# Kernel tuning notes

Hardware: AMD Instinct MI355X
Metric: run time of the kernel (lower is better)

The kernel has to match this reference:

```python
import jax, jax.numpy as jnp
import numpy as np

# EEACSF hyperparameters (module defaults)
CUTOFF = 5.2
ANG_CUTOFF = 3.5
RADIAL_ETA = 16.0
ANGULAR_ETA = 8.0
RDIV = 16          # radial_dist_divisions
ADIV = 4           # angular_dist_divisions
ZETA = 32.0
SECTIONS = 4       # angle_sections
R_START = 0.8
A_START = 0.8
N_SPECIES = 87     # size of periodic-table / valence table

N_ATOMS = 20000
N_EDGES = 640000       # radial edges
N_ANG_EDGES = 160000   # angular-graph edges
N_PAIRS = 560000       # angle pairs


def setup_inputs() -> dict:
    key = jax.random.key(0)
    ks = jax.random.split(key, 12)
    species = jax.random.randint(ks[0], (N_ATOMS,), 0, N_SPECIES)
    # radial graph: distances in (R_START, CUTOFF)
    distances = R_START + (CUTOFF - R_START) * jax.random.uniform(ks[1], (N_EDGES,), jnp.float32)
    switch = jax.random.uniform(ks[2], (N_EDGES,), jnp.float32)
    edge_src = jax.random.randint(ks[3], (N_EDGES,), 0, N_ATOMS)
    edge_dst = jax.random.randint(ks[4], (N_EDGES,), 0, N_ATOMS)
    # angular graph
    ang_angles = np.pi * jax.random.uniform(ks[5], (N_PAIRS,), jnp.float32)
    ang_distances = A_START + (ANG_CUTOFF - A_START) * jax.random.uniform(ks[6], (N_ANG_EDGES,), jnp.float32)
    ang_switch = jax.random.uniform(ks[7], (N_ANG_EDGES,), jnp.float32)
    ang_edge_dst = jax.random.randint(ks[8], (N_ANG_EDGES,), 0, N_ATOMS)
    angle_src = jax.random.randint(ks[9], (N_PAIRS,), 0, N_ANG_EDGES)
    angle_dst = jax.random.randint(ks[10], (N_PAIRS,), 0, N_ANG_EDGES)
    central_atom = jax.random.randint(ks[11], (N_PAIRS,), 0, N_ATOMS)
    # valence structure table (stands in for the preprocessed VALENCE_STRUCTURE constant)
    valence_table = jax.random.uniform(jax.random.fold_in(key, 99), (N_SPECIES, 4), jnp.float32)
    return {
        "species": species, "distances": distances, "switch": switch,
        "edge_src": edge_src, "edge_dst": edge_dst,
        "ang_angles": ang_angles, "ang_distances": ang_distances,
        "ang_switch": ang_switch, "ang_edge_dst": ang_edge_dst,
        "angle_src": angle_src, "angle_dst": angle_dst,
        "central_atom": central_atom, "valence_table": valence_table,
    }


def reference(species, distances, switch, edge_src, edge_dst,
              ang_angles, ang_distances, ang_switch, ang_edge_dst,
              angle_src, angle_dst, central_atom, valence_table):
    n_atoms = species.shape[0]
    valence = valence_table[species]                                  # [N,4]

    # ---- radial AEV ----
    shiftR = jnp.asarray(np.linspace(R_START, CUTOFF, RDIV + 1)[None, :-1], distances.dtype)
    x2 = RADIAL_ETA * (distances[:, None] - shiftR) ** 2              # [E,16]
    radial_terms = 0.25 * jnp.exp(-x2) * switch[:, None]              # [E,16]
    radial_aev = jax.ops.segment_sum(
        radial_terms[:, :, None] * valence[edge_dst, None, :],        # [E,16,4]
        edge_src, num_segments=n_atoms,
    ).reshape(n_atoms, -1)                                            # [N,64]

    # ---- angular AEV ----
    d12 = 0.5 * (ang_distances[angle_src] + ang_distances[angle_dst])[:, None]  # [P,1]
    angle_start = np.pi / (2 * SECTIONS)
    shiftZ = jnp.asarray((np.linspace(0, np.pi, SECTIONS + 1) + angle_start)[None, :-1], ang_distances.dtype)
    shiftA = jnp.asarray(np.linspace(A_START, ANG_CUTOFF, ADIV + 1)[None, :-1], ang_distances.dtype)
    factor1 = (0.5 + 0.5 * jnp.cos(ang_angles[:, None] - shiftZ)) ** ZETA       # [P,4]
    factor2 = jnp.exp(-ANGULAR_ETA * (d12 - shiftA) ** 2)                       # [P,4]
    angular_terms = (factor1[:, None, :] * factor2[:, :, None]).reshape(-1, SECTIONS * ADIV)
    angular_terms = angular_terms * 2 * (ang_switch[angle_src] * ang_switch[angle_dst])[:, None]  # [P,16]

    valence_dst = valence[ang_edge_dst]                               # [E2,4]
    vp = valence_dst[angle_src] + valence_dst[angle_dst]              # [P,4]
    vm = valence_dst[angle_src] * valence_dst[angle_dst]              # [P,4]
    valence_ang = (vp[:, :, None] * vm[:, None, :]).reshape(-1, 16)   # [P,16]

    angular_aev = jax.ops.segment_sum(
        angular_terms[:, :, None] * valence_ang[:, None, :],          # [P,16,16]
        central_atom, num_segments=n_atoms,
    ).reshape(n_atoms, -1)                                            # [N,256]

    onehot = jax.nn.one_hot(species, N_SPECIES, dtype=distances.dtype)  # [N,87]
    return jnp.concatenate((onehot, radial_aev, angular_aev), axis=-1)  # [N,407]
```

## Files before the change

### kernel.cpp

```cpp
#include <hip/hip_runtime.h>
#include <hip/hip_fp16.h>
#include <math.h>

#define NCOLS   407
#define RAD_OFF 87
#define ANG_OFF 151
#define T1      3072
#define KPT     (T1 / 256)
#define WB      32
#define MAXBKT  640
#define CAPF    1792
#define C2      (CAPF / 256)


typedef __attribute__((ext_vector_type(8))) _Float16 f16x8;
typedef __attribute__((ext_vector_type(4))) float    f32x4;

static __device__ inline unsigned pack2(float a, float b) {
    __half2 h = __floats2half2_rn(a, b);
    return *reinterpret_cast<unsigned*>(&h);
}
static __device__ inline float2 unpack2(unsigned u) {
    __half2 h = *reinterpret_cast<__half2*>(&u);
    return __half22float2(h);
}

__global__ __launch_bounds__(256) void ze_kernel(const float* __restrict__ ang_dist,
                                                 const float* __restrict__ ang_sw,
                                                 const int* __restrict__ ang_edge_dst,
                                                 const float* __restrict__ dist,
                                                 const float* __restrict__ sw,
                                                 const int* __restrict__ edst,
                                                 const int* __restrict__ species,
                                                 const float4* __restrict__ valence,
                                                 uint4* __restrict__ edata,
                                                 uint4* __restrict__ rad_edata,
                                                 int* __restrict__ cursors,
                                                 int n_ang_edges, int n_edges,
                                                 int nbe, int nbr) {
    int bid = blockIdx.x;
    int t = threadIdx.x;
    if (bid == nbe + nbr) {
        for (int i = t; i < 2 * MAXBKT; i += 256) cursors[i] = 0;
        return;
    }
    if (bid < nbe) {
        int i = bid * 2560 + t;
        #pragma unroll
        for (int k = 0; k < 10; ++k, i += 256) {
            if (i < n_ang_edges) {
                float4 v = valence[species[ang_edge_dst[i]]];
                uint4 r;
                r.x = __float_as_uint(ang_dist[i]);
                r.y = __float_as_uint(ang_sw[i]);
                r.z = pack2(v.x, v.y);
                r.w = pack2(v.z, v.w);
                edata[i] = r;
            }
        }
    } else {
        int i = (bid - nbe) * 2560 + t;
        #pragma unroll
        for (int k = 0; k < 10; ++k, i += 256) {
            if (i < n_edges) {
                float d  = dist[i];
                float ps = 0.25f * sw[i];
                float4 v = valence[species[edst[i]]];
                uint4 r;
                r.x = __float_as_uint(d);
                r.y = pack2(ps * v.x, ps * v.y);
                r.z = pack2(ps * v.z, ps * v.w);
                r.w = 0u;
                rad_edata[i] = r;
            }
        }
    }
}

__global__ __launch_bounds__(256) void pass1_kernel(
    const uint4* __restrict__ rad_edata,
    const int* __restrict__ esrc,
    const float* __restrict__ ang_angles,
    const int* __restrict__ psrc, const int* __restrict__ pdst,
    const int* __restrict__ central,
    int* __restrict__ cur_rad, int* __restrict__ cur_ang,
    uint4* __restrict__ arr_rad, uint4* __restrict__ arr_ang,
    int n_edges, int n_pairs, int nbkt, int nt_rad)
{
    __shared__ uint4 buf[T1];
    __shared__ int   lh[MAXBKT];
    __shared__ int   gb[MAXBKT];
    __shared__ int   wtot[4];

    int bid = blockIdx.x;
    int t = threadIdx.x;
    int is_ang = bid >= nt_rad;
    const int* key = is_ang ? central : esrc;
    int* cursor = is_ang ? cur_ang : cur_rad;
    int n   = is_ang ? n_pairs : n_edges;
    int off = (is_ang ? bid - nt_rad : bid) * T1;
    int cnt = min(T1, n - off);
    uint4* arr = is_ang ? arr_ang : arr_rad;

    for (int b = t; b < nbkt; b += 256) lh[b] = 0;
    __syncthreads();

    int meta[KPT];
    #pragma unroll
    for (int k = 0; k < KPT; ++k) {
        int i = off + k * 256 + t;
        meta[k] = -1;
        if (i < n) {
            int atom = key[i];
            int r = atomicAdd(&lh[atom >> 5], 1);
            meta[k] = (atom << 12) | r;
        }
    }
    __syncthreads();

    {
        int w = t >> 6, lane = t & 63;
        int W4  = (nbkt + 3) >> 2;
        int wlo = w * W4;
        int whi = min(wlo + W4, nbkt);
        int b0 = wlo + lane * 3;
        int c0 = (b0     < whi) ? lh[b0]     : 0;
        int c1 = (b0 + 1 < whi) ? lh[b0 + 1] : 0;
        int c2 = (b0 + 2 < whi) ? lh[b0 + 2] : 0;
        int lsum = c0 + c1 + c2;
        int s = lsum;
        #pragma unroll
        for (int o = 1; o < 64; o <<= 1) {
            int u = __shfl_up(s, o, 64);
            if (lane >= o) s += u;
        }
        int excl = s - lsum;
        if (c0) gb[b0]     = b0       * CAPF + atomicAdd(&cursor[b0],     c0);
        if (c1) gb[b0 + 1] = (b0 + 1) * CAPF + atomicAdd(&cursor[b0 + 1], c1);
        if (c2) gb[b0 + 2] = (b0 + 2) * CAPF + atomicAdd(&cursor[b0 + 2], c2);
        if (b0     < whi) lh[b0]     = excl;
        if (b0 + 1 < whi) lh[b0 + 1] = excl + c0;
        if (b0 + 2 < whi) lh[b0 + 2] = excl + c0 + c1;
        if (lane == 63) wtot[w] = s;
        __syncthreads();
        int wbase = 0;
        for (int ww = 0; ww < w; ++ww) wbase += wtot[ww];
        if (wbase) {
            if (b0     < whi) lh[b0]     += wbase;
            if (b0 + 1 < whi) lh[b0 + 1] += wbase;
            if (b0 + 2 < whi) lh[b0 + 2] += wbase;
        }
        __syncthreads();
    }

    #pragma unroll
    for (int k = 0; k < KPT; ++k) {
        if (meta[k] < 0) continue;
        int i = off + k * 256 + t;
        int atom = meta[k] >> 12, r = meta[k] & 4095;
        int b = atom >> 5;
        uint4 rec;
        if (!is_ang) {
            uint4 e = rad_edata[i];
            rec.x = e.x; rec.y = e.y; rec.z = e.z;
            rec.w = (unsigned)atom;
        } else {
            rec.x = (unsigned)psrc[i];
            rec.y = (unsigned)pdst[i];
            rec.z = __float_as_uint(ang_angles[i]);
            rec.w = (unsigned)atom;
        }
        buf[lh[b] + r] = rec;
    }
    __syncthreads();

    #pragma unroll
    for (int k = 0; k < KPT; ++k) {
        int j = k * 256 + t;
        if (j < cnt) {
            uint4 r = buf[j];
            int b = (int)(r.w >> 5);
            int gpos = gb[b] + (j - lh[b]);
            if (gpos < (b + 1) * CAPF) arr[gpos] = r;
        }
    }
}

__global__ __launch_bounds__(256) void pass2B_kernel(
    const uint4* __restrict__ arr_rad, const uint4* __restrict__ arr_ang,
    const uint4* __restrict__ edata,
    const int* __restrict__ cur_rad, const int* __restrict__ cur_ang,
    const int* __restrict__ species,
    float* __restrict__ out, int nbkt, int n_atoms)
{
    __shared__ uint4 buf[CAPF];
    __shared__ unsigned short ord[CAPF];
    __shared__ int lh[WB];
    __shared__ int sA[WB + 1];
    __shared__ uint4 stg[4][256];

    int bid = blockIdx.x;
    int t = threadIdx.x;
    int g = bid >= nbkt;
    int b = g ? bid - nbkt : bid;
    int lo  = b * CAPF;
    int cnt = min(g ? cur_ang[b] : cur_rad[b], CAPF);
    const uint4* arr = g ? arr_ang : arr_rad;
    int loA = b << 5;

    if (t < WB) lh[t] = 0;
    __syncthreads();
    int myar[C2];
    #pragma unroll
    for (int c = 0; c < C2; ++c) {
        int j = c * 256 + t;
        myar[c] = -1;
        if (j < cnt) {
            uint4 r = arr[lo + j];
            buf[j] = r;
            int a = (int)r.w - loA;
            if ((unsigned)a < WB) {
                int rk = atomicAdd(&lh[a], 1);
                myar[c] = (a << 12) | rk;
            }
        }
    }
    __syncthreads();
    if (t < 64) {
        int v = (t < WB) ? lh[t] : 0;
        int s = v;
        #pragma unroll
        for (int o = 1; o < WB; o <<= 1) {
            int u = __shfl_up(s, o, 64);
            if (t >= o) s += u;
        }
        if (t < WB) sA[t + 1] = s;
        if (t == 0) sA[0] = 0;
    }
    __syncthreads();
    #pragma unroll
    for (int c = 0; c < C2; ++c) {
        if (myar[c] >= 0) {
            int j = c * 256 + t;
            ord[sA[myar[c] >> 12] + (myar[c] & 4095)] = (unsigned short)j;
        }
    }
    __syncthreads();

    int w    = t >> 6;
    int lane = t & 63;
    int m  = lane & 15;
    int g4 = lane >> 4;

    if (g) {
        const _Float16* hl = (const _Float16*)stg[w];
        for (int ai = 0; ai < 8; ++ai) {
            int a = w * 8 + ai;
            int atom = loA + a;
            if (atom >= n_atoms) break;
            int beg = sA[a], end = sA[a + 1];
            f32x4 acc = {0.f, 0.f, 0.f, 0.f};

            for (int base = beg; base < end; base += 64) {
                int idx = base + lane;
                unsigned q[16];
                if (idx < end) {
                    uint4 pr = buf[ord[idx]];
                    int e1 = (int)pr.x;
                    int e2 = (int)pr.y;
                    float ang = __uint_as_float(pr.z);
                    uint4 r1 = edata[e1];
                    uint4 r2 = edata[e2];
                    float d12 = 0.5f * (__uint_as_float(r1.x) + __uint_as_float(r2.x));
                    float swp = 2.0f * __uint_as_float(r1.y) * __uint_as_float(r2.y);
                    float2 v1a = unpack2(r1.z), v1b = unpack2(r1.w);
                    float2 v2a = unpack2(r2.z), v2b = unpack2(r2.w);
                    float vp[4] = {v1a.x + v2a.x, v1a.y + v2a.y, v1b.x + v2b.x, v1b.y + v2b.y};
                    float vm[4] = {v1a.x * v2a.x, v1a.y * v2a.y, v1b.x * v2b.x, v1b.y * v2b.y};

                    float sa, ca;
                    __sincosf(ang, &sa, &ca);
                    const float czv[4] = { 0.92387953f,  0.38268343f, -0.38268343f, -0.92387953f };
                    const float szv[4] = { 0.38268343f,  0.92387953f,  0.92387953f,  0.38268343f };
                    float f1v[4];
                    #pragma unroll
                    for (int z = 0; z < 4; ++z) {
                        float y = 0.5f + 0.5f * (ca * czv[z] + sa * szv[z]);
                        float y2 = y * y, y4 = y2 * y2, y8 = y4 * y4, y16 = y8 * y8;
                        f1v[z] = y16 * y16;
                    }
                    float f2sv[4];
                    #pragma unroll
                    for (int aa = 0; aa < 4; ++aa) {
                        float x = d12 - (0.8f + 0.675f * (float)aa);
                        f2sv[aa] = swp * __expf(-8.0f * x * x);
                    }
                    #pragma unroll
                    for (int aa = 0; aa < 4; ++aa) {
                        q[aa * 2 + 0] = pack2(f2sv[aa] * f1v[0], f2sv[aa] * f1v[1]);
                        q[aa * 2 + 1] = pack2(f2sv[aa] * f1v[2], f2sv[aa] * f1v[3]);
                    }
                    #pragma unroll
                    for (int i2 = 0; i2 < 4; ++i2) {
                        q[8 + i2 * 2 + 0] = pack2(vp[i2] * vm[0], vp[i2] * vm[1]);
                        q[8 + i2 * 2 + 1] = pack2(vp[i2] * vm[2], vp[i2] * vm[3]);
                    }
                } else {
                    #pragma unroll
                    for (int k = 0; k < 16; ++k) q[k] = 0u;
                }
                stg[w][lane * 4 + 0] = make_uint4(q[0],  q[1],  q[2],  q[3]);
                stg[w][lane * 4 + 1] = make_uint4(q[4],  q[5],  q[6],  q[7]);
                stg[w][lane * 4 + 2] = make_uint4(q[8],  q[9],  q[10], q[11]);
                stg[w][lane * 4 + 3] = make_uint4(q[12], q[13], q[14], q[15]);
                asm volatile("s_waitcnt lgkmcnt(0)" ::: "memory");

                int cc = min(64, end - base);
                {
                    f16x8 wf, uf;
                    #pragma unroll
                    for (int i = 0; i < 8; ++i) {
                        int row = (g4 << 3) + i;
                        wf[i] = hl[row * 32 + m];
                        uf[i] = hl[row * 32 + 16 + m];
                    }
                    acc = __builtin_amdgcn_mfma_f32_16x16x32_f16(wf, uf, acc, 0, 0, 0);
                }
                if (cc > 32) {
                    f16x8 wf, uf;
                    #pragma unroll
                    for (int i = 0; i < 8; ++i) {
                        int row = 32 + (g4 << 3) + i;
                        wf[i] = hl[row * 32 + m];
                        uf[i] = hl[row * 32 + 16 + m];
                    }
                    acc = __builtin_amdgcn_mfma_f32_16x16x32_f16(wf, uf, acc, 0, 0, 0);
                }
                asm volatile("s_waitcnt lgkmcnt(0)" ::: "memory");
            }
            float* orow = out + (size_t)atom * NCOLS + ANG_OFF;
            #pragma unroll
            for (int r = 0; r < 4; ++r)
                orow[(g4 * 4 + r) * 16 + m] = acc[r];
        }
        return;
    }

    const _Float16* hl = (const _Float16*)buf;
    const float*    fl = (const float*)buf;
    float shiftm = 0.8f + 0.275f * (float)m;
    for (int ai = 0; ai < 8; ++ai) {
        int a = w * 8 + ai;
        int atom = loA + a;
        if (atom >= n_atoms) break;
        int beg = sA[a], end = sA[a + 1];
        f32x4 acc = {0.f, 0.f, 0.f, 0.f};

        for (int base = beg; base < end; base += 64) {
            int cnt2 = min(64, end - base);
            {
                f16x8 wf, uf;
                #pragma unroll
                for (int i = 0; i < 8; ++i) {
                    int k = (g4 << 3) + i;
                    int live = (k < cnt2);
                    int o = live ? (int)ord[base + k] : 0;
                    float d = fl[o * 4];
                    float x = d - shiftm;
                    float e = __expf(-16.0f * x * x);
                    wf[i] = live ? (_Float16)e : (_Float16)0.0f;
                    uf[i] = (live && m < 4) ? hl[o * 8 + 2 + m] : (_Float16)0.0f;
                }
                acc = __builtin_amdgcn_mfma_f32_16x16x32_f16(wf, uf, acc, 0, 0, 0);
            }
            if (cnt2 > 32) {
                f16x8 wf, uf;
                #pragma unroll
                for (int i = 0; i < 8; ++i) {
                    int k = 32 + (g4 << 3) + i;
                    int live = (k < cnt2);
                    int o = live ? (int)ord[base + k] : 0;
                    float d = fl[o * 4];
                    float x = d - shiftm;
                    float e = __expf(-16.0f * x * x);
                    wf[i] = live ? (_Float16)e : (_Float16)0.0f;
                    uf[i] = (live && m < 4) ? hl[o * 8 + 2 + m] : (_Float16)0.0f;
                }
                acc = __builtin_amdgcn_mfma_f32_16x16x32_f16(wf, uf, acc, 0, 0, 0);
            }
        }
        if (m < 4) {
            size_t rowbase = (size_t)atom * NCOLS;
            #pragma unroll
            for (int r = 0; r < 4; ++r)
                out[rowbase + RAD_OFF + (g4 * 4 + r) * 4 + m] = acc[r];
        }
    }

    for (int idx2 = t; idx2 < WB * 87; idx2 += 256) {
        int a = idx2 / 87, c = idx2 - a * 87;
        int atom = loA + a;
        if (atom < n_atoms)
            out[(size_t)atom * NCOLS + c] = (c == species[atom]) ? 1.0f : 0.0f;
    }
}

extern "C" void kernel_launch(void* const* d_in, const int* in_sizes, int n_in,
                              void* d_out, int out_size, void* d_ws, size_t ws_size,
                              hipStream_t stream) {
    const int*   species      = (const int*)  d_in[0];
    const float* distances    = (const float*)d_in[1];
    const float* switch_      = (const float*)d_in[2];
    const int*   edge_src     = (const int*)  d_in[3];
    const int*   edge_dst     = (const int*)  d_in[4];
    const float* ang_angles   = (const float*)d_in[5];
    const float* ang_dist     = (const float*)d_in[6];
    const float* ang_switch   = (const float*)d_in[7];
    const int*   ang_edge_dst = (const int*)  d_in[8];
    const int*   angle_src    = (const int*)  d_in[9];
    const int*   angle_dst    = (const int*)  d_in[10];
    const int*   central_atom = (const int*)  d_in[11];
    const float4* valence     = (const float4*)d_in[12];

    float* out = (float*)d_out;

    const int n_atoms     = in_sizes[0];
    const int n_edges     = in_sizes[1];
    const int n_ang_edges = in_sizes[6];
    const int n_pairs     = in_sizes[5];

    const int nbkt   = (n_atoms + WB - 1) / WB;
    const int nt_rad = (n_edges + T1 - 1) / T1;
    const int nt_ang = (n_pairs + T1 - 1) / T1;

    char* ws = (char*)d_ws;
    size_t off = 0;
    auto alloc = [&](size_t bytes) -> void* {
        void* p = ws + off;
        off = (off + bytes + 15) & ~(size_t)15;
        return p;
    };
    uint4* arr_rad   = (uint4*)alloc((size_t)nbkt * CAPF * 16);
    uint4* arr_ang   = (uint4*)alloc((size_t)nbkt * CAPF * 16);
    uint4* rad_edata = (uint4*)alloc((size_t)n_edges * 16);
    uint4* edata     = (uint4*)alloc((size_t)n_ang_edges * 16);
    int*   cursors   = (int*)  alloc((size_t)2 * MAXBKT * sizeof(int));
    int* cur_rad = cursors;
    int* cur_ang = cursors + MAXBKT;

    int nbe = (n_ang_edges + 2559) / 2560;
    int nbr = (n_edges + 2559) / 2560;
    ze_kernel<<<nbe + nbr + 1, 256, 0, stream>>>(
        ang_dist, ang_switch, ang_edge_dst, distances, switch_, edge_dst,
        species, valence, edata, rad_edata, cursors,
        n_ang_edges, n_edges, nbe, nbr);

    pass1_kernel<<<nt_rad + nt_ang, 256, 0, stream>>>(
        rad_edata, edge_src, ang_angles, angle_src, angle_dst, central_atom,
        cur_rad, cur_ang, arr_rad, arr_ang,
        n_edges, n_pairs, nbkt, nt_rad);

    pass2B_kernel<<<2 * nbkt, 256, 0, stream>>>(
        arr_rad, arr_ang, edata, cur_rad, cur_ang, species, out, nbkt, n_atoms);
}
```

Baseline: 80.23 us.

## Pack angle pairs of a wave's eight atoms into shared 64-lane chunks

The angular path used to process each of a wave's eight atoms separately, padding each atom's pair list up to 64 lanes. It now streams the concatenated pair range of all eight atoms in full 64-lane chunks and masks MFMA rows per atom, flushing an atom's accumulator when its segment ends. This cuts idle lanes and wasted feature evaluations when atoms have few pairs (about 28 on average). In exchange it adds per-chunk segment bookkeeping and can issue extra MFMAs when a 32-row block spans several atoms.

```diff
diff --git a/kernel.cpp b/kernel.cpp
--- a/kernel.cpp
+++ b/kernel.cpp
@@ -254,94 +254,111 @@
 
     if (g) {
         const _Float16* hl = (const _Float16*)stg[w];
-        for (int ai = 0; ai < 8; ++ai) {
-            int a = w * 8 + ai;
-            int atom = loA + a;
-            if (atom >= n_atoms) break;
-            int beg = sA[a], end = sA[a + 1];
-            f32x4 acc = {0.f, 0.f, 0.f, 0.f};
-
-            for (int base = beg; base < end; base += 64) {
-                int idx = base + lane;
-                unsigned q[16];
-                if (idx < end) {
-                    uint4 pr = buf[ord[idx]];
-                    int e1 = (int)pr.x;
-                    int e2 = (int)pr.y;
-                    float ang = __uint_as_float(pr.z);
-                    uint4 r1 = edata[e1];
-                    uint4 r2 = edata[e2];
-                    float d12 = 0.5f * (__uint_as_float(r1.x) + __uint_as_float(r2.x));
-                    float swp = 2.0f * __uint_as_float(r1.y) * __uint_as_float(r2.y);
-                    float2 v1a = unpack2(r1.z), v1b = unpack2(r1.w);
-                    float2 v2a = unpack2(r2.z), v2b = unpack2(r2.w);
-                    float vp[4] = {v1a.x + v2a.x, v1a.y + v2a.y, v1b.x + v2b.x, v1b.y + v2b.y};
-                    float vm[4] = {v1a.x * v2a.x, v1a.y * v2a.y, v1b.x * v2b.x, v1b.y * v2b.y};
-
-                    float sa, ca;
-                    __sincosf(ang, &sa, &ca);
-                    const float czv[4] = { 0.92387953f,  0.38268343f, -0.38268343f, -0.92387953f };
-                    const float szv[4] = { 0.38268343f,  0.92387953f,  0.92387953f,  0.38268343f };
-                    float f1v[4];
-                    #pragma unroll
-                    for (int z = 0; z < 4; ++z) {
-                        float y = 0.5f + 0.5f * (ca * czv[z] + sa * szv[z]);
-                        float y2 = y * y, y4 = y2 * y2, y8 = y4 * y4, y16 = y8 * y8;
-                        f1v[z] = y16 * y16;
+        int aw0 = w * 8;
+        int R0 = sA[aw0], R1 = sA[aw0 + 8];
+        int cur = aw0;
+        f32x4 acc = {0.f, 0.f, 0.f, 0.f};
+
+        for (int base = R0; base < R1; base += 64) {
+            int idx = base + lane;
+            unsigned q[16];
+            if (idx < R1) {
+                uint4 pr = buf[ord[idx]];
+                int e1 = (int)pr.x;
+                int e2 = (int)pr.y;
+                float ang = __uint_as_float(pr.z);
+                uint4 r1 = edata[e1];
+                uint4 r2 = edata[e2];
+                float d12 = 0.5f * (__uint_as_float(r1.x) + __uint_as_float(r2.x));
+                float swp = 2.0f * __uint_as_float(r1.y) * __uint_as_float(r2.y);
+                float2 v1a = unpack2(r1.z), v1b = unpack2(r1.w);
+                float2 v2a = unpack2(r2.z), v2b = unpack2(r2.w);
+                float vp[4] = {v1a.x + v2a.x, v1a.y + v2a.y, v1b.x + v2b.x, v1b.y + v2b.y};
+                float vm[4] = {v1a.x * v2a.x, v1a.y * v2a.y, v1b.x * v2b.x, v1b.y * v2b.y};
+
+                float sa, ca;
+                __sincosf(ang, &sa, &ca);
+                const float czv[4] = { 0.92387953f,  0.38268343f, -0.38268343f, -0.92387953f };
+                const float szv[4] = { 0.38268343f,  0.92387953f,  0.92387953f,  0.38268343f };
+                float f1v[4];
+                #pragma unroll
+                for (int z = 0; z < 4; ++z) {
+                    float y = 0.5f + 0.5f * (ca * czv[z] + sa * szv[z]);
+                    float y2 = y * y, y4 = y2 * y2, y8 = y4 * y4, y16 = y8 * y8;
+                    f1v[z] = y16 * y16;
+                }
+                float f2sv[4];
+                #pragma unroll
+                for (int aa = 0; aa < 4; ++aa) {
+                    float x = d12 - (0.8f + 0.675f * (float)aa);
+                    f2sv[aa] = swp * __expf(-8.0f * x * x);
+                }
+                #pragma unroll
+                for (int aa = 0; aa < 4; ++aa) {
+                    q[aa * 2 + 0] = pack2(f2sv[aa] * f1v[0], f2sv[aa] * f1v[1]);
+                    q[aa * 2 + 1] = pack2(f2sv[aa] * f1v[2], f2sv[aa] * f1v[3]);
+                }
+                #pragma unroll
+                for (int i2 = 0; i2 < 4; ++i2) {
+                    q[8 + i2 * 2 + 0] = pack2(vp[i2] * vm[0], vp[i2] * vm[1]);
+                    q[8 + i2 * 2 + 1] = pack2(vp[i2] * vm[2], vp[i2] * vm[3]);
+                }
+            } else {
+                #pragma unroll
+                for (int k = 0; k < 16; ++k) q[k] = 0u;
+            }
+            stg[w][lane * 4 + 0] = make_uint4(q[0],  q[1],  q[2],  q[3]);
+            stg[w][lane * 4 + 1] = make_uint4(q[4],  q[5],  q[6],  q[7]);
+            stg[w][lane * 4 + 2] = make_uint4(q[8],  q[9],  q[10], q[11]);
+            stg[w][lane * 4 + 3] = make_uint4(q[12], q[13], q[14], q[15]);
+            asm volatile("s_waitcnt lgkmcnt(0)" ::: "memory");
+
+            #pragma unroll
+            for (int c = 0; c < 2; ++c) {
+                int cbase = base + c * 32;
+                if (cbase >= R1) break;
+                while (cur < aw0 + 8) {
+                    int abeg = sA[cur], aend = sA[cur + 1];
+                    int lo_r = max(abeg, cbase) - cbase;
+                    int hi_r = min(aend, cbase + 32) - cbase;
+                    if (hi_r > lo_r) {
+                        f16x8 wf, uf;
+                        #pragma unroll
+                        for (int i = 0; i < 8; ++i) {
+                            int rr  = (g4 << 3) + i;
+                            int row = c * 32 + rr;
+                            bool live = (rr >= lo_r && rr < hi_r);
+                            wf[i] = live ? hl[row * 32 + m] : (_Float16)0.0f;
+                            uf[i] = hl[row * 32 + 16 + m];
+                        }
+                        acc = __builtin_amdgcn_mfma_f32_16x16x32_f16(wf, uf, acc, 0, 0, 0);
                     }
-                    float f2sv[4];
-                    #pragma unroll
-                    for (int aa = 0; aa < 4; ++aa) {
-                        float x = d12 - (0.8f + 0.675f * (float)aa);
-                        f2sv[aa] = swp * __expf(-8.0f * x * x);
+                    if (aend <= cbase + 32) {
+                        int atom = loA + cur;
+                        if (atom < n_atoms) {
+                            float* orow = out + (size_t)atom * NCOLS + ANG_OFF;
+                            #pragma unroll
+                            for (int r = 0; r < 4; ++r)
+                                orow[(g4 * 4 + r) * 16 + m] = acc[r];
+                        }
+                        acc = (f32x4){0.f, 0.f, 0.f, 0.f};
+                        ++cur;
+                    } else {
+                        break;
                     }
-                    #pragma unroll
-                    for (int aa = 0; aa < 4; ++aa) {
-                        q[aa * 2 + 0] = pack2(f2sv[aa] * f1v[0], f2sv[aa] * f1v[1]);
-                        q[aa * 2 + 1] = pack2(f2sv[aa] * f1v[2], f2sv[aa] * f1v[3]);
-                    }
-                    #pragma unroll
-                    for (int i2 = 0; i2 < 4; ++i2) {
-                        q[8 + i2 * 2 + 0] = pack2(vp[i2] * vm[0], vp[i2] * vm[1]);
-                        q[8 + i2 * 2 + 1] = pack2(vp[i2] * vm[2], vp[i2] * vm[3]);
-                    }
-                } else {
-                    #pragma unroll
-                    for (int k = 0; k < 16; ++k) q[k] = 0u;
-                }
-                stg[w][lane * 4 + 0] = make_uint4(q[0],  q[1],  q[2],  q[3]);
-                stg[w][lane * 4 + 1] = make_uint4(q[4],  q[5],  q[6],  q[7]);
-                stg[w][lane * 4 + 2] = make_uint4(q[8],  q[9],  q[10], q[11]);
-                stg[w][lane * 4 + 3] = make_uint4(q[12], q[13], q[14], q[15]);
-                asm volatile("s_waitcnt lgkmcnt(0)" ::: "memory");
-
-                int cc = min(64, end - base);
-                {
-                    f16x8 wf, uf;
-                    #pragma unroll
-                    for (int i = 0; i < 8; ++i) {
-                        int row = (g4 << 3) + i;
-                        wf[i] = hl[row * 32 + m];
-                        uf[i] = hl[row * 32 + 16 + m];
-                    }
-                    acc = __builtin_amdgcn_mfma_f32_16x16x32_f16(wf, uf, acc, 0, 0, 0);
-                }
-                if (cc > 32) {
-                    f16x8 wf, uf;
-                    #pragma unroll
-                    for (int i = 0; i < 8; ++i) {
-                        int row = 32 + (g4 << 3) + i;
-                        wf[i] = hl[row * 32 + m];
-                        uf[i] = hl[row * 32 + 16 + m];
-                    }
-                    acc = __builtin_amdgcn_mfma_f32_16x16x32_f16(wf, uf, acc, 0, 0, 0);
-                }
-                asm volatile("s_waitcnt lgkmcnt(0)" ::: "memory");
-            }
-            float* orow = out + (size_t)atom * NCOLS + ANG_OFF;
-            #pragma unroll
-            for (int r = 0; r < 4; ++r)
-                orow[(g4 * 4 + r) * 16 + m] = acc[r];
+                }
+            }
+            asm volatile("s_waitcnt lgkmcnt(0)" ::: "memory");
+        }
+        while (cur < aw0 + 8) {
+            int atom = loA + cur;
+            if (atom < n_atoms) {
+                float* orow = out + (size_t)atom * NCOLS + ANG_OFF;
+                #pragma unroll
+                for (int r = 0; r < 4; ++r)
+                    orow[(g4 * 4 + r) * 16 + m] = 0.0f;
+            }
+            ++cur;
         }
         return;
     }
```

New measurement: 80.56 us. Within noise of the previous version (+0.4%).
